# Performance work log

Measured on AMD Instinct MI355X. Metric: run time of the kernel, lower is better.

The kernel has to match this reference:

```python
import jax, jax.numpy as jnp
import numpy as np

SMOOTH = 1.0

def setup_inputs() -> dict:
    key = jax.random.key(0)
    k1, k2 = jax.random.split(key)
    pred = jax.random.uniform(k1, (64, 1, 512, 512), dtype=jnp.float32)
    target = jax.random.randint(k2, (64, 1, 512, 512), 0, 2).astype(jnp.float32)
    # make a few rows all-zero to exercise the zero-mask branch
    target = target.at[:4].set(0.0)
    return {"pred": pred, "target": target}

def reference(pred, target):
    B = pred.shape[0]
    p = pred.astype(jnp.float32).reshape(B, -1)   # [B, N]
    t = target.astype(jnp.float32).reshape(B, -1)  # [B, N]
    t_sum = jnp.sum(t, axis=1)                     # [B]
    p_sum = jnp.sum(p, axis=1)                     # [B]
    inter = jnp.sum(p * t, axis=1)                 # [B]
    dice = (2.0 * inter + SMOOTH) / (p_sum + t_sum + SMOOTH)
    dice_loss = 1.0 - dice
    zero_loss = p_sum / p.shape[1]                 # pred_row.mean()
    losses = jnp.where(t_sum == 0, zero_loss, dice_loss)
    return jnp.mean(losses)
```

## Files before the change

kernel.cpp:

```cpp
#include <hip/hip_runtime.h>

#define N_PER_BATCH (512 * 512)
#define BLOCKS_PER_BATCH 32
#define NBATCH 64
#define THREADS 256

__global__ __launch_bounds__(THREADS) void dice_stage1(
    const float* __restrict__ pred, const float* __restrict__ tgt,
    float* __restrict__ partial) {
    const int b  = blockIdx.x >> 5;
    const int cb = blockIdx.x & 31;

    const float4* p4 = reinterpret_cast<const float4*>(pred + (size_t)b * N_PER_BATCH);
    const float4* t4 = reinterpret_cast<const float4*>(tgt  + (size_t)b * N_PER_BATCH);

    const int base = cb * (N_PER_BATCH / BLOCKS_PER_BATCH / 4);

    float4 p[8], t[8];
#pragma unroll
    for (int i = 0; i < 8; ++i) p[i] = p4[base + i * THREADS + threadIdx.x];
#pragma unroll
    for (int i = 0; i < 8; ++i) t[i] = t4[base + i * THREADS + threadIdx.x];

    float ps = 0.f, ts = 0.f, is = 0.f;
#pragma unroll
    for (int i = 0; i < 8; ++i) {
        ps += (p[i].x + p[i].y) + (p[i].z + p[i].w);
        ts += (t[i].x + t[i].y) + (t[i].z + t[i].w);
        is += (p[i].x * t[i].x + p[i].y * t[i].y) + (p[i].z * t[i].z + p[i].w * t[i].w);
    }

#pragma unroll
    for (int off = 32; off > 0; off >>= 1) {
        ps += __shfl_down(ps, off, 64);
        ts += __shfl_down(ts, off, 64);
        is += __shfl_down(is, off, 64);
    }

    __shared__ float s[3][4];
    const int wid  = threadIdx.x >> 6;
    const int lane = threadIdx.x & 63;
    if (lane == 0) { s[0][wid] = ps; s[1][wid] = ts; s[2][wid] = is; }
    __syncthreads();
    if (threadIdx.x == 0) {
        const float P = (s[0][0] + s[0][1]) + (s[0][2] + s[0][3]);
        const float T = (s[1][0] + s[1][1]) + (s[1][2] + s[1][3]);
        const float I = (s[2][0] + s[2][1]) + (s[2][2] + s[2][3]);
        float* o = partial + ((size_t)b * BLOCKS_PER_BATCH + cb) * 3;
        o[0] = P; o[1] = T; o[2] = I;
    }
}

__global__ __launch_bounds__(64) void dice_stage2(
    const float* __restrict__ partial, float* __restrict__ out) {
    const int b = threadIdx.x;
    float P = 0.f, T = 0.f, I = 0.f;
#pragma unroll
    for (int i = 0; i < BLOCKS_PER_BATCH; ++i) {
        const float* p = partial + ((size_t)b * BLOCKS_PER_BATCH + i) * 3;
        P += p[0]; T += p[1]; I += p[2];
    }
    const float dice_loss = 1.0f - (2.0f * I + 1.0f) / (P + T + 1.0f);
    const float zero_loss = P / (float)N_PER_BATCH;
    float loss = (T == 0.0f) ? zero_loss : dice_loss;
#pragma unroll
    for (int off = 32; off > 0; off >>= 1) loss += __shfl_down(loss, off, 64);
    if (b == 0) out[0] = loss * (1.0f / (float)NBATCH);
}

extern "C" void kernel_launch(void* const* d_in, const int* in_sizes, int n_in,
                              void* d_out, int out_size, void* d_ws, size_t ws_size,
                              hipStream_t stream) {
    const float* pred = (const float*)d_in[0];
    const float* tgt  = (const float*)d_in[1];
    float* out = (float*)d_out;
    float* partial = (float*)d_ws;

    dice_stage1<<<NBATCH * BLOCKS_PER_BATCH, THREADS, 0, stream>>>(pred, tgt, partial);
    dice_stage2<<<1, 64, 0, stream>>>(partial, out);
}
```

Before: 26.44 us.

## Fuse two-stage dice reduction into one kernel with last-block atomic finalize

Merges the second reduction kernel into the first. Each block publishes its partials and bumps a global atomic counter, and the last block to arrive does the final per-batch sums and loss computation. The partials are also laid out batch-contiguous per chunk so the final reads coalesce. This removes the second kernel launch and its gap, but adds a memset launch to reset the counter plus atomic traffic on every block.

```diff
diff --git a/kernel.cpp b/kernel.cpp
--- a/kernel.cpp
+++ b/kernel.cpp
@@ -4,16 +4,17 @@
 #define BLOCKS_PER_BATCH 32
 #define NBATCH 64
 #define THREADS 256
+#define GRID (NBATCH * BLOCKS_PER_BATCH)
 
-__global__ __launch_bounds__(THREADS) void dice_stage1(
+
+__global__ __launch_bounds__(THREADS) void dice_fused(
     const float* __restrict__ pred, const float* __restrict__ tgt,
-    float* __restrict__ partial) {
+    float* __restrict__ ws, float* __restrict__ out) {
     const int b  = blockIdx.x >> 5;
     const int cb = blockIdx.x & 31;
 
     const float4* p4 = reinterpret_cast<const float4*>(pred + (size_t)b * N_PER_BATCH);
     const float4* t4 = reinterpret_cast<const float4*>(tgt  + (size_t)b * N_PER_BATCH);
-
     const int base = cb * (N_PER_BATCH / BLOCKS_PER_BATCH / 4);
 
     float4 p[8], t[8];
@@ -38,34 +39,57 @@
     }
 
     __shared__ float s[3][4];
+    __shared__ int amLast;
     const int wid  = threadIdx.x >> 6;
     const int lane = threadIdx.x & 63;
     if (lane == 0) { s[0][wid] = ps; s[1][wid] = ts; s[2][wid] = is; }
     __syncthreads();
+
+    unsigned* counter = reinterpret_cast<unsigned*>(ws);
+    float* P = ws + 64;
+    float* T = P + GRID;
+    float* I = T + GRID;
+
     if (threadIdx.x == 0) {
-        const float P = (s[0][0] + s[0][1]) + (s[0][2] + s[0][3]);
-        const float T = (s[1][0] + s[1][1]) + (s[1][2] + s[1][3]);
-        const float I = (s[2][0] + s[2][1]) + (s[2][2] + s[2][3]);
-        float* o = partial + ((size_t)b * BLOCKS_PER_BATCH + cb) * 3;
-        o[0] = P; o[1] = T; o[2] = I;
+        const float Pv = (s[0][0] + s[0][1]) + (s[0][2] + s[0][3]);
+        const float Tv = (s[1][0] + s[1][1]) + (s[1][2] + s[1][3]);
+        const float Iv = (s[2][0] + s[2][1]) + (s[2][2] + s[2][3]);
+        const int idx = cb * NBATCH + b;
+        __hip_atomic_store(&P[idx], Pv, __ATOMIC_RELAXED, __HIP_MEMORY_SCOPE_AGENT);
+        __hip_atomic_store(&T[idx], Tv, __ATOMIC_RELAXED, __HIP_MEMORY_SCOPE_AGENT);
+        __hip_atomic_store(&I[idx], Iv, __ATOMIC_RELAXED, __HIP_MEMORY_SCOPE_AGENT);
+        const unsigned old = __hip_atomic_fetch_add(counter, 1u, __ATOMIC_ACQ_REL,
+                                                    __HIP_MEMORY_SCOPE_AGENT);
+        amLast = (old == GRID - 1) ? 1 : 0;
     }
-}
+    __syncthreads();
+    if (!amLast) return;
 
-__global__ __launch_bounds__(64) void dice_stage2(
-    const float* __restrict__ partial, float* __restrict__ out) {
-    const int b = threadIdx.x;
-    float P = 0.f, T = 0.f, I = 0.f;
+    __hip_atomic_fetch_add(counter, 0u, __ATOMIC_ACQUIRE, __HIP_MEMORY_SCOPE_AGENT);
+
+    const int g = threadIdx.x >> 6;
+    float Pb = 0.f, Tb = 0.f, Ib = 0.f;
 #pragma unroll
-    for (int i = 0; i < BLOCKS_PER_BATCH; ++i) {
-        const float* p = partial + ((size_t)b * BLOCKS_PER_BATCH + i) * 3;
-        P += p[0]; T += p[1]; I += p[2];
+    for (int c = 0; c < 8; ++c) {
+        const int idx = (g * 8 + c) * NBATCH + lane;
+        Pb += __hip_atomic_load(&P[idx], __ATOMIC_RELAXED, __HIP_MEMORY_SCOPE_AGENT);
+        Tb += __hip_atomic_load(&T[idx], __ATOMIC_RELAXED, __HIP_MEMORY_SCOPE_AGENT);
+        Ib += __hip_atomic_load(&I[idx], __ATOMIC_RELAXED, __HIP_MEMORY_SCOPE_AGENT);
     }
-    const float dice_loss = 1.0f - (2.0f * I + 1.0f) / (P + T + 1.0f);
-    const float zero_loss = P / (float)N_PER_BATCH;
-    float loss = (T == 0.0f) ? zero_loss : dice_loss;
+    __shared__ float r[3][4][64];
+    r[0][g][lane] = Pb; r[1][g][lane] = Tb; r[2][g][lane] = Ib;
+    __syncthreads();
+    if (threadIdx.x < 64) {
+        const float Ps = (r[0][0][lane] + r[0][1][lane]) + (r[0][2][lane] + r[0][3][lane]);
+        const float Ts = (r[1][0][lane] + r[1][1][lane]) + (r[1][2][lane] + r[1][3][lane]);
+        const float Is = (r[2][0][lane] + r[2][1][lane]) + (r[2][2][lane] + r[2][3][lane]);
+        const float dice_loss = 1.0f - (2.0f * Is + 1.0f) / (Ps + Ts + 1.0f);
+        const float zero_loss = Ps / (float)N_PER_BATCH;
+        float loss = (Ts == 0.0f) ? zero_loss : dice_loss;
 #pragma unroll
-    for (int off = 32; off > 0; off >>= 1) loss += __shfl_down(loss, off, 64);
-    if (b == 0) out[0] = loss * (1.0f / (float)NBATCH);
+        for (int off = 32; off > 0; off >>= 1) loss += __shfl_down(loss, off, 64);
+        if (lane == 0) out[0] = loss * (1.0f / (float)NBATCH);
+    }
 }
 
 extern "C" void kernel_launch(void* const* d_in, const int* in_sizes, int n_in,
@@ -74,8 +98,8 @@
     const float* pred = (const float*)d_in[0];
     const float* tgt  = (const float*)d_in[1];
     float* out = (float*)d_out;
-    float* partial = (float*)d_ws;
+    float* ws  = (float*)d_ws;
 
-    dice_stage1<<<NBATCH * BLOCKS_PER_BATCH, THREADS, 0, stream>>>(pred, tgt, partial);
-    dice_stage2<<<1, 64, 0, stream>>>(partial, out);
+    hipMemsetAsync(d_ws, 0, sizeof(unsigned), stream);
+    dice_fused<<<GRID, THREADS, 0, stream>>>(pred, tgt, ws, out);
 }
```

Result: slower. 94.64 us (+257.9%).

## Fuse two-stage dice reduction into one kernel with last-block atomic counters

Applied to the files above, without the earlier changes.

Replaces the separate stage-2 kernel with a last-block-done pattern. Each block publishes its partials, bumps a per-batch counter, and the final block per batch computes that batch's loss. A global counter then lets the last batch finisher average all losses. This removes one kernel launch and its dependency gap, but adds a hipMemsetAsync to clear the counters each call, plus atomics and relaxed memory-ordering risk.

```diff
diff --git a/kernel.cpp b/kernel.cpp
--- a/kernel.cpp
+++ b/kernel.cpp
@@ -1,20 +1,29 @@
 #include <hip/hip_runtime.h>
 
 #define N_PER_BATCH (512 * 512)
-#define BLOCKS_PER_BATCH 32
+#define BPB 32
 #define NBATCH 64
 #define THREADS 256
+#define GRID (NBATCH * BPB)
 
-__global__ __launch_bounds__(THREADS) void dice_stage1(
+
+#define L1_STRIDE_U32 16
+#define L2_OFF_U32    1024
+#define LOSS_OFF      1088
+#define P_OFF         1280
+#define T_OFF         (P_OFF + GRID)
+#define I_OFF         (T_OFF + GRID)
+#define CLEAR_BYTES   4160
+
+__global__ __launch_bounds__(THREADS) void dice_fused(
     const float* __restrict__ pred, const float* __restrict__ tgt,
-    float* __restrict__ partial) {
+    float* __restrict__ ws, float* __restrict__ out) {
     const int b  = blockIdx.x >> 5;
     const int cb = blockIdx.x & 31;
 
     const float4* p4 = reinterpret_cast<const float4*>(pred + (size_t)b * N_PER_BATCH);
     const float4* t4 = reinterpret_cast<const float4*>(tgt  + (size_t)b * N_PER_BATCH);
-
-    const int base = cb * (N_PER_BATCH / BLOCKS_PER_BATCH / 4);
+    const int base = cb * (N_PER_BATCH / BPB / 4);
 
     float4 p[8], t[8];
 #pragma unroll
@@ -38,34 +47,66 @@
     }
 
     __shared__ float s[3][4];
-    const int wid  = threadIdx.x >> 6;
-    const int lane = threadIdx.x & 63;
-    if (lane == 0) { s[0][wid] = ps; s[1][wid] = ts; s[2][wid] = is; }
+    __shared__ int sLast;
+    {
+        const int wid  = threadIdx.x >> 6;
+        const int lane = threadIdx.x & 63;
+        if (lane == 0) { s[0][wid] = ps; s[1][wid] = ts; s[2][wid] = is; }
+    }
     __syncthreads();
+
+    unsigned* u = reinterpret_cast<unsigned*>(ws);
+
     if (threadIdx.x == 0) {
-        const float P = (s[0][0] + s[0][1]) + (s[0][2] + s[0][3]);
-        const float T = (s[1][0] + s[1][1]) + (s[1][2] + s[1][3]);
-        const float I = (s[2][0] + s[2][1]) + (s[2][2] + s[2][3]);
-        float* o = partial + ((size_t)b * BLOCKS_PER_BATCH + cb) * 3;
-        o[0] = P; o[1] = T; o[2] = I;
+        const float Pv = (s[0][0] + s[0][1]) + (s[0][2] + s[0][3]);
+        const float Tv = (s[1][0] + s[1][1]) + (s[1][2] + s[1][3]);
+        const float Iv = (s[2][0] + s[2][1]) + (s[2][2] + s[2][3]);
+        const int idx = b * BPB + cb;
+        __hip_atomic_store(&ws[P_OFF + idx], Pv, __ATOMIC_RELAXED, __HIP_MEMORY_SCOPE_AGENT);
+        __hip_atomic_store(&ws[T_OFF + idx], Tv, __ATOMIC_RELAXED, __HIP_MEMORY_SCOPE_AGENT);
+        __hip_atomic_store(&ws[I_OFF + idx], Iv, __ATOMIC_RELAXED, __HIP_MEMORY_SCOPE_AGENT);
+        asm volatile("s_waitcnt vmcnt(0)" ::: "memory");
+        const unsigned old = __hip_atomic_fetch_add(&u[b * L1_STRIDE_U32], 1u,
+                                                    __ATOMIC_RELAXED, __HIP_MEMORY_SCOPE_AGENT);
+        sLast = (old == BPB - 1) ? 1 : 0;
     }
-}
+    __syncthreads();
+    if (!sLast) return;
+    if (threadIdx.x >= 64) return;
 
-__global__ __launch_bounds__(64) void dice_stage2(
-    const float* __restrict__ partial, float* __restrict__ out) {
-    const int b = threadIdx.x;
-    float P = 0.f, T = 0.f, I = 0.f;
+    const int lane = threadIdx.x;
+    float pv = 0.f, tv = 0.f, iv = 0.f;
+    if (lane < BPB) {
+        const int idx = b * BPB + lane;
+        pv = __hip_atomic_load(&ws[P_OFF + idx], __ATOMIC_RELAXED, __HIP_MEMORY_SCOPE_AGENT);
+        tv = __hip_atomic_load(&ws[T_OFF + idx], __ATOMIC_RELAXED, __HIP_MEMORY_SCOPE_AGENT);
+        iv = __hip_atomic_load(&ws[I_OFF + idx], __ATOMIC_RELAXED, __HIP_MEMORY_SCOPE_AGENT);
+    }
 #pragma unroll
-    for (int i = 0; i < BLOCKS_PER_BATCH; ++i) {
-        const float* p = partial + ((size_t)b * BLOCKS_PER_BATCH + i) * 3;
-        P += p[0]; T += p[1]; I += p[2];
+    for (int off = 16; off > 0; off >>= 1) {
+        pv += __shfl_down(pv, off, 64);
+        tv += __shfl_down(tv, off, 64);
+        iv += __shfl_down(iv, off, 64);
     }
-    const float dice_loss = 1.0f - (2.0f * I + 1.0f) / (P + T + 1.0f);
-    const float zero_loss = P / (float)N_PER_BATCH;
-    float loss = (T == 0.0f) ? zero_loss : dice_loss;
+
+    int last2flag = 0;
+    if (lane == 0) {
+        const float dice_loss = 1.0f - (2.0f * iv + 1.0f) / (pv + tv + 1.0f);
+        const float zero_loss = pv / (float)N_PER_BATCH;
+        const float loss_b = (tv == 0.0f) ? zero_loss : dice_loss;
+        __hip_atomic_store(&ws[LOSS_OFF + b], loss_b, __ATOMIC_RELAXED, __HIP_MEMORY_SCOPE_AGENT);
+        asm volatile("s_waitcnt vmcnt(0)" ::: "memory");
+        const unsigned old2 = __hip_atomic_fetch_add(&u[L2_OFF_U32], 1u,
+                                                     __ATOMIC_RELAXED, __HIP_MEMORY_SCOPE_AGENT);
+        last2flag = (old2 == NBATCH - 1) ? 1 : 0;
+    }
+    const int last2 = __shfl(last2flag, 0, 64);
+    if (!last2) return;
+
+    float l = __hip_atomic_load(&ws[LOSS_OFF + lane], __ATOMIC_RELAXED, __HIP_MEMORY_SCOPE_AGENT);
 #pragma unroll
-    for (int off = 32; off > 0; off >>= 1) loss += __shfl_down(loss, off, 64);
-    if (b == 0) out[0] = loss * (1.0f / (float)NBATCH);
+    for (int off = 32; off > 0; off >>= 1) l += __shfl_down(l, off, 64);
+    if (lane == 0) out[0] = l * (1.0f / (float)NBATCH);
 }
 
 extern "C" void kernel_launch(void* const* d_in, const int* in_sizes, int n_in,
@@ -74,8 +115,8 @@
     const float* pred = (const float*)d_in[0];
     const float* tgt  = (const float*)d_in[1];
     float* out = (float*)d_out;
-    float* partial = (float*)d_ws;
+    float* ws  = (float*)d_ws;
 
-    dice_stage1<<<NBATCH * BLOCKS_PER_BATCH, THREADS, 0, stream>>>(pred, tgt, partial);
-    dice_stage2<<<1, 64, 0, stream>>>(partial, out);
+    hipMemsetAsync(d_ws, 0, CLEAR_BYTES, stream);
+    dice_fused<<<GRID, THREADS, 0, stream>>>(pred, tgt, ws, out);
 }
```

New measurement: 32.16 us. 1.22x slower.
